# Kernel optimization log

Hardware: AMD Instinct MI355X
Metric: run time of the kernel (lower is better)

Reference implementation:

```python
import jax, jax.numpy as jnp
import numpy as np

DIM = 1024
HEADS = 16
HEAD_DIM = DIM // HEADS
SCALE = HEAD_DIM ** -0.5
LN_EPS = 1e-5


def setup_inputs() -> dict:
    key = jax.random.key(0)
    ks = jax.random.split(key, 8)
    B, N = 2, 2048
    s = 0.02
    return {
        "embedding1": jax.random.normal(ks[0], (B, N, DIM), jnp.float32),
        "embedding2": jax.random.normal(ks[1], (B, N, DIM), jnp.float32),
        "Wqkv": jax.random.normal(ks[2], (DIM, 3 * DIM), jnp.float32) * s,
        "bqkv": jnp.zeros((3 * DIM,), jnp.float32),
        "Wout": jax.random.normal(ks[3], (DIM, DIM), jnp.float32) * s,
        "bout": jnp.zeros((DIM,), jnp.float32),
        "gamma": jnp.ones((DIM,), jnp.float32),
        "beta": jnp.zeros((DIM,), jnp.float32),
    }


def _layernorm(x, gamma, beta):
    mu = jnp.mean(x, axis=-1, keepdims=True)
    var = jnp.mean(jnp.square(x - mu), axis=-1, keepdims=True)
    return (x - mu) * jax.lax.rsqrt(var + LN_EPS) * gamma + beta


def _qkv(x, Wqkv, bqkv):
    B, N, _ = x.shape
    qkv = (x @ Wqkv + bqkv).reshape(B, N, 3, HEADS, HEAD_DIM)
    return qkv[:, :, 0], qkv[:, :, 1], qkv[:, :, 2]  # each [B,N,H,D]


def _cross_attn(q, k, v):
    # q: [B,N,H,D], k/v: [B,S,H,D]
    scores = jnp.einsum("bnhd,bshd->bhns", q, k) * SCALE
    attn = jax.nn.softmax(scores, axis=-1)
    out = jnp.einsum("bhns,bshd->bnhd", attn, v)
    B, N = out.shape[0], out.shape[1]
    return out.reshape(B, N, DIM)


def reference(embedding1, embedding2, Wqkv, bqkv, Wout, bout, gamma, beta):
    q1, k1, v1 = _qkv(embedding1, Wqkv, bqkv)
    q2, k2, v2 = _qkv(embedding2, Wqkv, bqkv)
    attn1 = _cross_attn(q1, k2, v2)
    attn2 = _cross_attn(q2, k1, v1)
    out1 = _layernorm(embedding1 + attn1 @ Wout + bout, gamma, beta)
    out2 = _layernorm(embedding2 + attn2 @ Wout + bout, gamma, beta)
    return (out1, out2)
```

## Files before the change

### kernel.cpp

```cpp
#include <hip/hip_runtime.h>
#include <stdint.h>
#include <stddef.h>

#define DIM 1024
#define HEADS 16
#define HDIM 64
#define NTOK 2048

typedef __attribute__((ext_vector_type(8))) __bf16 bf16x8;
typedef __attribute__((ext_vector_type(4))) float f32x4;
typedef __attribute__((ext_vector_type(16))) float f32x16;
typedef __attribute__((ext_vector_type(4))) short short4v;
typedef __attribute__((ext_vector_type(4))) uint32_t u32x4;

__device__ __forceinline__ short f2bs(float f) {
  uint32_t u = __builtin_bit_cast(uint32_t, f);
  uint32_t r = (u + 0x7FFFu + ((u >> 16) & 1u)) >> 16;
  return (short)r;
}

__device__ __forceinline__ uint32_t cvtpk(float lo, float hi) {
  uint32_t r;
  asm("v_cvt_pk_bf16_f32 %0, %1, %2" : "=v"(r) : "v"(lo), "v"(hi));
  return r;
}

__device__ __forceinline__ f32x4 MFMA(bf16x8 a, bf16x8 b, f32x4 c) {
  return __builtin_amdgcn_mfma_f32_16x16x32_bf16(a, b, c, 0, 0, 0);
}
__device__ __forceinline__ f32x16 MFMA32(bf16x8 a, bf16x8 b, f32x16 c) {
  return __builtin_amdgcn_mfma_f32_32x32x16_bf16(a, b, c, 0, 0, 0);
}

__device__ __forceinline__ void gl_lds16(const void* g, void* l) {
  __builtin_amdgcn_global_load_lds(
      (const __attribute__((address_space(1))) void*)g,
      (__attribute__((address_space(3))) void*)l, 16, 0, 0);
}

__global__ __launch_bounds__(256) void cast_embs(const float4* __restrict__ e1,
                                                 const float4* __restrict__ e2,
                                                 short* __restrict__ X) {
  int i = blockIdx.x * 256 + threadIdx.x;
  const int half4 = (4096 * 1024) / 4;
  float4 v = (i < half4) ? e1[i] : e2[i - half4];
  short4v o;
  o.x = f2bs(v.x); o.y = f2bs(v.y); o.z = f2bs(v.z); o.w = f2bs(v.w);
  *(short4v*)&X[(size_t)i * 4] = o;
}

__global__ __launch_bounds__(256) void transpose_cast(const float* __restrict__ W,
                                                      short* __restrict__ Wt,
                                                      int R, int C) {
  __shared__ float tile[32][33];
  int tx = threadIdx.x, ty = threadIdx.y;
  int c0 = blockIdx.x * 32, r0 = blockIdx.y * 32;
#pragma unroll
  for (int i = 0; i < 32; i += 8)
    tile[ty + i][tx] = W[(size_t)(r0 + ty + i) * C + c0 + tx];
  __syncthreads();
#pragma unroll
  for (int i = 0; i < 32; i += 8)
    Wt[(size_t)(c0 + ty + i) * R + r0 + tx] = f2bs(tile[tx][ty + i]);
}

template <int EPI>
__global__ __launch_bounds__(256, 2) void gemm_bt(
    const short* __restrict__ A, const short* __restrict__ Bt, int K,
    const float* __restrict__ bias,
    const float* __restrict__ e1, const float* __restrict__ e2,
    short* __restrict__ oq, short* __restrict__ okk, short* __restrict__ ovt,
    float* __restrict__ oy) {
  __shared__ short lA[128 * 32];
  __shared__ short lB[128 * 32];
  int tid = threadIdx.x;
  int l = tid & 63, w = tid >> 6;
  int wr = w >> 1, wc = w & 1;
  int row0 = blockIdx.x * 128, col0 = blockIdx.y * 128;
  f32x4 acc[4][4] = {};

  for (int kk = 0; kk < K; kk += 32) {
#pragma unroll
    for (int i = 0; i < 2; i++) {
      int f = i * 256 + tid;
      int r = f >> 2, cb = (f & 3) * 8;
      gl_lds16(A + (size_t)(row0 + r) * K + kk + cb, (char*)lA + (size_t)f * 16);
      gl_lds16(Bt + (size_t)(col0 + r) * K + kk + cb, (char*)lB + (size_t)f * 16);
    }
    __syncthreads();
    bf16x8 af[4], bfr[4];
#pragma unroll
    for (int mi = 0; mi < 4; mi++)
      af[mi] = *(const bf16x8*)&lA[(wr * 64 + mi * 16 + (l & 15)) * 32 + (l >> 4) * 8];
#pragma unroll
    for (int ni = 0; ni < 4; ni++)
      bfr[ni] = *(const bf16x8*)&lB[(wc * 64 + ni * 16 + (l & 15)) * 32 + (l >> 4) * 8];
#pragma unroll
    for (int mi = 0; mi < 4; mi++)
#pragma unroll
      for (int ni = 0; ni < 4; ni++)
        acc[mi][ni] = MFMA(af[mi], bfr[ni], acc[mi][ni]);
    __syncthreads();
  }

#pragma unroll
  for (int mi = 0; mi < 4; mi++) {
#pragma unroll
    for (int ni = 0; ni < 4; ni++) {
#pragma unroll
      for (int r = 0; r < 4; r++) {
        int grow = row0 + wr * 64 + mi * 16 + (l >> 4) * 4 + r;
        int gcol = col0 + wc * 64 + ni * 16 + (l & 15);
        float v = acc[mi][ni][r] + bias[gcol];
        if (EPI == 0) {
          int t = gcol >> 10, rem = gcol & 1023;
          int h = rem >> 6, d = rem & 63;
          int e = grow >> 12, b = (grow >> 11) & 1, n = grow & 2047;
          size_t ebh = (size_t)((e * 2 + b) * 16 + h) * (NTOK * HDIM);
          if (t == 0) {
            oq[ebh + (size_t)n * HDIM + d] = f2bs(v * 0.18033688f);
          } else if (t == 1) {
            int ks = d >> 4, hi2 = (d >> 3) & 1, j = d & 7;
            int tt = n >> 6, rr = n & 63, h2 = rr >> 5, lo = rr & 31;
            okk[ebh + (((size_t)(tt * 8 + ks * 2 + h2)) * 64 + hi2 * 32 + lo) * 8 + j] = f2bs(v);
          } else {
            int tt = n >> 6, rr = n & 63;
            int ks = rr >> 4, hi2 = (rr >> 3) & 1, j = rr & 7;
            int h2 = d >> 5, lo = d & 31;
            ovt[ebh + (((size_t)(tt * 8 + ks * 2 + h2)) * 64 + hi2 * 32 + lo) * 8 + j] = f2bs(v);
          }
        } else {
          float res = (grow < 4096) ? e1[(size_t)grow * DIM + gcol]
                                    : e2[(size_t)(grow - 4096) * DIM + gcol];
          oy[(size_t)grow * DIM + gcol] = v + res;
        }
      }
    }
  }
}

__global__ __launch_bounds__(64, 2) void attn_kernel(
    const short* __restrict__ qbuf, const short* __restrict__ kfb,
    const short* __restrict__ vfb, short* __restrict__ X2) {
  int phys = blockIdx.x;
  int work = (phys & 7) * 256 + (phys >> 3);
  int qw = work & 31;
  int inst = work >> 5;
  int h = inst & 15, b = (inst >> 4) & 1, a = inst >> 5;
  int l = threadIdx.x;
  int lo5 = l & 31, hi = l >> 5;

  size_t qo = (size_t)((a * 2 + b) * 16 + h) * (NTOK * HDIM);
  size_t ko = (size_t)(((a ^ 1) * 2 + b) * 16 + h) * (NTOK * HDIM);
  const short* Q = qbuf + qo;
  const short* Kf = kfb + ko;
  const short* Vf = vfb + ko;
  int qrowA = qw * 64 + lo5;
  int qrowB = qrowA + 32;

  bf16x8 qfA[4], qfB[4];
#pragma unroll
  for (int ks = 0; ks < 4; ks++) {
    qfA[ks] = *(const bf16x8*)&Q[(size_t)qrowA * HDIM + hi * 8 + ks * 16];
    qfB[ks] = *(const bf16x8*)&Q[(size_t)qrowB * HDIM + hi * 8 + ks * 16];
  }

  f32x16 oA0 = {}, oA1 = {}, oB0 = {}, oB1 = {};
  float lsA = 0.f, lsB = 0.f;

  bf16x8 ka[8], va[8];

#define LOADF(dst, buf, t)                                                   \
  {                                                                          \
    const short* _p = &buf[((size_t)(t) * 8) * 512 + l * 8];                 \
    _Pragma("unroll") for (int fi = 0; fi < 8; fi++)                         \
        dst[fi] = *(const bf16x8*)&_p[fi * 512];                             \
  }

#define QKBLK(s0, s1, qf)                                                    \
  {                                                                          \
    __builtin_amdgcn_s_setprio(1);                                           \
    _Pragma("unroll") for (int ks = 0; ks < 4; ks++) {                       \
      s0 = MFMA32(ka[2 * ks], qf[ks], s0);                                   \
      s1 = MFMA32(ka[2 * ks + 1], qf[ks], s1);                               \
    }                                                                        \
    __builtin_amdgcn_s_setprio(0);                                           \
  }

#define SOFTPV(s0, s1, oo0, oo1, ls)                                         \
  {                                                                          \
    _Pragma("unroll") for (int i = 0; i < 16; i++) {                         \
      s0[i] = exp2f(s0[i]);                                                  \
      s1[i] = exp2f(s1[i]);                                                  \
    }                                                                        \
    {                                                                        \
      float rt[16];                                                          \
      _Pragma("unroll") for (int i = 0; i < 16; i++) rt[i] = s0[i] + s1[i];  \
      _Pragma("unroll") for (int sd = 8; sd >= 1; sd >>= 1)                  \
          _Pragma("unroll") for (int i = 0; i < sd; i++) rt[i] += rt[i + sd];\
      ls += rt[0];                                                           \
    }                                                                        \
    bf16x8 pf[4];                                                            \
    _Pragma("unroll") for (int ks = 0; ks < 4; ks++) {                       \
      const int rb = (ks & 1) * 8;                                           \
      uint32_t A0, A1, B0, B1;                                               \
      if (ks < 2) {                                                          \
        A0 = cvtpk(s0[rb + 0], s0[rb + 1]);                                  \
        A1 = cvtpk(s0[rb + 2], s0[rb + 3]);                                  \
        B0 = cvtpk(s0[rb + 4], s0[rb + 5]);                                  \
        B1 = cvtpk(s0[rb + 6], s0[rb + 7]);                                  \
      } else {                                                               \
        A0 = cvtpk(s1[rb + 0], s1[rb + 1]);                                  \
        A1 = cvtpk(s1[rb + 2], s1[rb + 3]);                                  \
        B0 = cvtpk(s1[rb + 4], s1[rb + 5]);                                  \
        B1 = cvtpk(s1[rb + 6], s1[rb + 7]);                                  \
      }                                                                      \
      asm("v_permlane32_swap_b32 %0, %1" : "+v"(A0), "+v"(B0));              \
      asm("v_permlane32_swap_b32 %0, %1" : "+v"(A1), "+v"(B1));              \
      u32x4 fw; fw.x = A0; fw.y = A1; fw.z = B0; fw.w = B1;                  \
      pf[ks] = __builtin_bit_cast(bf16x8, fw);                               \
    }                                                                        \
    __builtin_amdgcn_s_setprio(1);                                           \
    _Pragma("unroll") for (int ks = 0; ks < 4; ks++) {                       \
      oo0 = MFMA32(va[2 * ks], pf[ks], oo0);                                 \
      oo1 = MFMA32(va[2 * ks + 1], pf[ks], oo1);                             \
    }                                                                        \
    __builtin_amdgcn_s_setprio(0);                                           \
  }

  LOADF(ka, Kf, 0);
  LOADF(va, Vf, 0);
  for (int t = 0; t < 32; t++) {
    f32x16 sA0 = {}, sA1 = {};
    QKBLK(sA0, sA1, qfA);
    SOFTPV(sA0, sA1, oA0, oA1, lsA);
    f32x16 sB0 = {}, sB1 = {};
    QKBLK(sB0, sB1, qfB);
    LOADF(ka, Kf, (t + 1) & 31);
    SOFTPV(sB0, sB1, oB0, oB1, lsB);
    LOADF(va, Vf, (t + 1) & 31);
  }

  lsA += __shfl_xor(lsA, 32);
  lsB += __shfl_xor(lsB, 32);
  float invA = 1.f / lsA, invB = 1.f / lsB;
  size_t obaseA = (size_t)(a * 4096 + b * 2048 + qrowA) * DIM + h * HDIM;
  size_t obaseB = (size_t)(a * 4096 + b * 2048 + qrowB) * DIM + h * HDIM;
#pragma unroll
  for (int g = 0; g < 4; g++) {
    short4v s4;
    s4.x = f2bs(oA0[4 * g + 0] * invA);
    s4.y = f2bs(oA0[4 * g + 1] * invA);
    s4.z = f2bs(oA0[4 * g + 2] * invA);
    s4.w = f2bs(oA0[4 * g + 3] * invA);
    *(short4v*)&X2[obaseA + 8 * g + 4 * hi] = s4;
    s4.x = f2bs(oA1[4 * g + 0] * invA);
    s4.y = f2bs(oA1[4 * g + 1] * invA);
    s4.z = f2bs(oA1[4 * g + 2] * invA);
    s4.w = f2bs(oA1[4 * g + 3] * invA);
    *(short4v*)&X2[obaseA + 32 + 8 * g + 4 * hi] = s4;
    s4.x = f2bs(oB0[4 * g + 0] * invB);
    s4.y = f2bs(oB0[4 * g + 1] * invB);
    s4.z = f2bs(oB0[4 * g + 2] * invB);
    s4.w = f2bs(oB0[4 * g + 3] * invB);
    *(short4v*)&X2[obaseB + 8 * g + 4 * hi] = s4;
    s4.x = f2bs(oB1[4 * g + 0] * invB);
    s4.y = f2bs(oB1[4 * g + 1] * invB);
    s4.z = f2bs(oB1[4 * g + 2] * invB);
    s4.w = f2bs(oB1[4 * g + 3] * invB);
    *(short4v*)&X2[obaseB + 32 + 8 * g + 4 * hi] = s4;
  }
#undef LOADF
#undef QKBLK
#undef SOFTPV
}

__global__ __launch_bounds__(256) void ln_kernel(const float* __restrict__ Y,
                                                 const float* __restrict__ gamma,
                                                 const float* __restrict__ beta,
                                                 float* __restrict__ out) {
  int row = blockIdx.x, t = threadIdx.x;
  const float4 v = *(const float4*)&Y[(size_t)row * DIM + t * 4];
  float s = v.x + v.y + v.z + v.w;
  float s2 = v.x * v.x + v.y * v.y + v.z * v.z + v.w * v.w;
#pragma unroll
  for (int d = 1; d < 64; d <<= 1) { s += __shfl_xor(s, d); s2 += __shfl_xor(s2, d); }
  __shared__ float sb[8];
  int w = t >> 6, l = t & 63;
  if (l == 0) { sb[w] = s; sb[4 + w] = s2; }
  __syncthreads();
  s = sb[0] + sb[1] + sb[2] + sb[3];
  s2 = sb[4] + sb[5] + sb[6] + sb[7];
  float mu = s * (1.f / DIM);
  float var = s2 * (1.f / DIM) - mu * mu;
  float rr = rsqrtf(var + 1e-5f);
  const float4 g = *(const float4*)&gamma[t * 4];
  const float4 bb = *(const float4*)&beta[t * 4];
  float4 ov;
  ov.x = (v.x - mu) * rr * g.x + bb.x;
  ov.y = (v.y - mu) * rr * g.y + bb.y;
  ov.z = (v.z - mu) * rr * g.z + bb.z;
  ov.w = (v.w - mu) * rr * g.w + bb.w;
  *(float4*)&out[(size_t)row * DIM + t * 4] = ov;
}

extern "C" void kernel_launch(void* const* d_in, const int* in_sizes, int n_in,
                              void* d_out, int out_size, void* d_ws, size_t ws_size,
                              hipStream_t stream) {
  const float* e1 = (const float*)d_in[0];
  const float* e2 = (const float*)d_in[1];
  const float* Wqkv = (const float*)d_in[2];
  const float* bqkv = (const float*)d_in[3];
  const float* Wout = (const float*)d_in[4];
  const float* bout = (const float*)d_in[5];
  const float* gamma = (const float*)d_in[6];
  const float* beta = (const float*)d_in[7];

  char* p = (char*)d_ws;
  short* Xbf   = (short*)p;
  short* Wqkvt = (short*)(p + 16777216);
  short* Woutt = (short*)(p + 23068672);
  short* qbf   = (short*)(p + 25165824);
  short* kbf   = (short*)(p + 41943040);
  short* vtf   = (short*)(p + 58720256);
  float* Yres  = (float*)(p + 25165824);
  short* X2    = Xbf;
  float* out   = (float*)d_out;

  cast_embs<<<8192, 256, 0, stream>>>((const float4*)e1, (const float4*)e2, Xbf);
  transpose_cast<<<dim3(3072 / 32, 1024 / 32), dim3(32, 8), 0, stream>>>(Wqkv, Wqkvt, 1024, 3072);
  transpose_cast<<<dim3(1024 / 32, 1024 / 32), dim3(32, 8), 0, stream>>>(Wout, Woutt, 1024, 1024);
  gemm_bt<0><<<dim3(64, 24), 256, 0, stream>>>(Xbf, Wqkvt, 1024, bqkv,
                                               nullptr, nullptr, qbf, kbf, vtf, nullptr);
  attn_kernel<<<2048, 64, 0, stream>>>(qbf, kbf, vtf, X2);
  gemm_bt<1><<<dim3(64, 8), 256, 0, stream>>>(X2, Woutt, 1024, bout,
                                              e1, e2, nullptr, nullptr, nullptr, Yres);
  ln_kernel<<<8192, 256, 0, stream>>>(Yres, gamma, beta, out);
}
```

Measured before the change: 333.3 us.

## Double GEMM K-tile to 64 and store pre-LayerNorm residual in bf16

The GEMM main loop now stages 64-wide K slices instead of 32, which halves the number of barrier pairs and lets the loads feeding 32 MFMAs be issued together. Separately, the output-projection epilogue writes the residual sum as bf16 rather than fp32, and the LayerNorm kernel reads bf16. This halves the traffic of that intermediate tensor. In exchange, LDS use per block doubles, which may affect occupancy, and the output loses precision because LayerNorm statistics are computed on bf16-rounded values.

Measured after the change: 328.9 us. About the same (-1.3%).

```diff
diff --git a/kernel.cpp b/kernel.cpp
--- a/kernel.cpp
+++ b/kernel.cpp
@@ -17,6 +17,10 @@
   uint32_t u = __builtin_bit_cast(uint32_t, f);
   uint32_t r = (u + 0x7FFFu + ((u >> 16) & 1u)) >> 16;
   return (short)r;
+}
+
+__device__ __forceinline__ float bs2f(short s) {
+  return __builtin_bit_cast(float, (uint32_t)((uint16_t)s) << 16);
 }
 
 __device__ __forceinline__ uint32_t cvtpk(float lo, float hi) {
@@ -70,36 +74,41 @@
     const float* __restrict__ bias,
     const float* __restrict__ e1, const float* __restrict__ e2,
     short* __restrict__ oq, short* __restrict__ okk, short* __restrict__ ovt,
-    float* __restrict__ oy) {
-  __shared__ short lA[128 * 32];
-  __shared__ short lB[128 * 32];
+    short* __restrict__ oy) {
+  __shared__ short lA[128 * 64];
+  __shared__ short lB[128 * 64];
   int tid = threadIdx.x;
   int l = tid & 63, w = tid >> 6;
   int wr = w >> 1, wc = w & 1;
   int row0 = blockIdx.x * 128, col0 = blockIdx.y * 128;
   f32x4 acc[4][4] = {};
 
-  for (int kk = 0; kk < K; kk += 32) {
-#pragma unroll
-    for (int i = 0; i < 2; i++) {
+  for (int kk = 0; kk < K; kk += 64) {
+#pragma unroll
+    for (int i = 0; i < 4; i++) {
       int f = i * 256 + tid;
-      int r = f >> 2, cb = (f & 3) * 8;
+      int r = f >> 3, cb = (f & 7) * 8;
       gl_lds16(A + (size_t)(row0 + r) * K + kk + cb, (char*)lA + (size_t)f * 16);
       gl_lds16(Bt + (size_t)(col0 + r) * K + kk + cb, (char*)lB + (size_t)f * 16);
     }
     __syncthreads();
-    bf16x8 af[4], bfr[4];
-#pragma unroll
-    for (int mi = 0; mi < 4; mi++)
-      af[mi] = *(const bf16x8*)&lA[(wr * 64 + mi * 16 + (l & 15)) * 32 + (l >> 4) * 8];
-#pragma unroll
-    for (int ni = 0; ni < 4; ni++)
-      bfr[ni] = *(const bf16x8*)&lB[(wc * 64 + ni * 16 + (l & 15)) * 32 + (l >> 4) * 8];
-#pragma unroll
-    for (int mi = 0; mi < 4; mi++)
+    bf16x8 af[2][4], bfr[2][4];
+#pragma unroll
+    for (int k2 = 0; k2 < 2; k2++) {
+#pragma unroll
+      for (int mi = 0; mi < 4; mi++)
+        af[k2][mi] = *(const bf16x8*)&lA[(wr * 64 + mi * 16 + (l & 15)) * 64 + k2 * 32 + (l >> 4) * 8];
 #pragma unroll
       for (int ni = 0; ni < 4; ni++)
-        acc[mi][ni] = MFMA(af[mi], bfr[ni], acc[mi][ni]);
+        bfr[k2][ni] = *(const bf16x8*)&lB[(wc * 64 + ni * 16 + (l & 15)) * 64 + k2 * 32 + (l >> 4) * 8];
+    }
+#pragma unroll
+    for (int k2 = 0; k2 < 2; k2++)
+#pragma unroll
+      for (int mi = 0; mi < 4; mi++)
+#pragma unroll
+        for (int ni = 0; ni < 4; ni++)
+          acc[mi][ni] = MFMA(af[k2][mi], bfr[k2][ni], acc[mi][ni]);
     __syncthreads();
   }
 
@@ -132,7 +141,7 @@
         } else {
           float res = (grow < 4096) ? e1[(size_t)grow * DIM + gcol]
                                     : e2[(size_t)(grow - 4096) * DIM + gcol];
-          oy[(size_t)grow * DIM + gcol] = v + res;
+          oy[(size_t)grow * DIM + gcol] = f2bs(v + res);
         }
       }
     }
@@ -275,14 +284,15 @@
 #undef SOFTPV
 }
 
-__global__ __launch_bounds__(256) void ln_kernel(const float* __restrict__ Y,
+__global__ __launch_bounds__(256) void ln_kernel(const short* __restrict__ Y,
                                                  const float* __restrict__ gamma,
                                                  const float* __restrict__ beta,
                                                  float* __restrict__ out) {
   int row = blockIdx.x, t = threadIdx.x;
-  const float4 v = *(const float4*)&Y[(size_t)row * DIM + t * 4];
-  float s = v.x + v.y + v.z + v.w;
-  float s2 = v.x * v.x + v.y * v.y + v.z * v.z + v.w * v.w;
+  const short4v v4 = *(const short4v*)&Y[(size_t)row * DIM + t * 4];
+  float vx = bs2f(v4.x), vy = bs2f(v4.y), vz = bs2f(v4.z), vw = bs2f(v4.w);
+  float s = vx + vy + vz + vw;
+  float s2 = vx * vx + vy * vy + vz * vz + vw * vw;
 #pragma unroll
   for (int d = 1; d < 64; d <<= 1) { s += __shfl_xor(s, d); s2 += __shfl_xor(s2, d); }
   __shared__ float sb[8];
@@ -297,10 +307,10 @@
   const float4 g = *(const float4*)&gamma[t * 4];
   const float4 bb = *(const float4*)&beta[t * 4];
   float4 ov;
-  ov.x = (v.x - mu) * rr * g.x + bb.x;
-  ov.y = (v.y - mu) * rr * g.y + bb.y;
-  ov.z = (v.z - mu) * rr * g.z + bb.z;
-  ov.w = (v.w - mu) * rr * g.w + bb.w;
+  ov.x = (vx - mu) * rr * g.x + bb.x;
+  ov.y = (vy - mu) * rr * g.y + bb.y;
+  ov.z = (vz - mu) * rr * g.z + bb.z;
+  ov.w = (vw - mu) * rr * g.w + bb.w;
   *(float4*)&out[(size_t)row * DIM + t * 4] = ov;
 }
 
@@ -323,7 +333,7 @@
   short* qbf   = (short*)(p + 25165824);
   short* kbf   = (short*)(p + 41943040);
   short* vtf   = (short*)(p + 58720256);
-  float* Yres  = (float*)(p + 25165824);
+  short* Yres  = (short*)(p + 25165824);
   short* X2    = Xbf;
   float* out   = (float*)d_out;
 
```
